# Kernel tuning notes

Hardware: AMD Instinct MI355X
Metric: run time of the kernel (lower is better)

Reference implementation:

```python
import jax, jax.numpy as jnp
import numpy as np

NB = 8            # num_blocks
D = 128           # embed_dim
D_INNER = 256     # expand=2
HEADS = 4
P = 64            # headdim
N = 32            # d_state
K = 4             # d_conv
CONV_DIM = D_INNER + 2 * N          # 320 (x, B, C streams)
D_IN_PROJ = 2 * D_INNER + 2 * N + HEADS  # 580 (z, xBC, dt)


def setup_inputs():
    key = jax.random.key(0)
    ks = iter(jax.random.split(key, 16))
    f = lambda shape, s=0.02: (jax.random.normal(next(ks), shape, jnp.float32) * s)
    B, L = 2, 4096
    return {
        'x': jax.random.normal(next(ks), (B, L, D), jnp.float32),
        'residual': jnp.zeros((B, L, D), jnp.float32),
        'ln1_w': jnp.ones((NB, D)), 'ln1_b': jnp.zeros((NB, D)),
        'ln2_w': jnp.ones((NB, D)), 'ln2_b': jnp.zeros((NB, D)),
        'fc1_w': f((NB, 4 * D, D)), 'fc1_b': jnp.zeros((NB, 4 * D)),
        'fc2_w': f((NB, D, 2 * D)), 'fc2_b': jnp.zeros((NB, D)),
        'in_proj_w': f((NB, D_IN_PROJ, D)),
        'conv_w': f((NB, CONV_DIM, K), 0.1), 'conv_b': jnp.zeros((NB, CONV_DIM)),
        'dt_bias': f((NB, HEADS), 0.1),
        'A_log': jnp.tile(jnp.log(jnp.arange(1, HEADS + 1, dtype=jnp.float32)), (NB, 1)),
        'Dp': jnp.ones((NB, HEADS)),
        'rms_w': jnp.ones((NB, D_INNER)),
        'out_proj_w': f((NB, D, D_INNER)),
        'h': 64, 'w': 64,
    }


def layernorm(x, w, b):
    mu = jnp.mean(x, -1, keepdims=True)
    var = jnp.mean((x - mu) ** 2, -1, keepdims=True)
    return (x - mu) * jax.lax.rsqrt(var + 1e-5) * w + b


def mamba2(x, in_proj_w, conv_w, conv_b, dt_bias, A_log, Dp, rms_w, out_proj_w):
    Bb, L, _ = x.shape
    zxbcdt = jnp.einsum('bld,ed->ble', x, in_proj_w)          # [B,L,580]
    z = zxbcdt[..., :D_INNER]
    xBC = zxbcdt[..., D_INNER:D_INNER + CONV_DIM]
    dt = jax.nn.softplus(zxbcdt[..., -HEADS:] + dt_bias)      # [B,L,H]
    # causal depthwise conv1d + silu
    xc = jnp.moveaxis(xBC, 1, 2)                              # [B,C,L]
    xc = jax.lax.conv_general_dilated(xc, conv_w[:, None, :], (1,), [(K - 1, 0)],
                                      feature_group_count=CONV_DIM)
    xBC = jax.nn.silu(jnp.moveaxis(xc, 1, 2) + conv_b)
    xs = xBC[..., :D_INNER].reshape(Bb, L, HEADS, P)          # [B,L,H,P]
    Bm = xBC[..., D_INNER:D_INNER + N]                        # [B,L,N]
    Cm = xBC[..., D_INNER + N:]                               # [B,L,N]
    dA = jnp.exp(dt * (-jnp.exp(A_log)))                      # [B,L,H]

    def step(hst, inp):
        dA_t, dt_t, B_t, C_t, x_t = inp
        hst = hst * dA_t[:, :, None, None] + (dt_t[:, :, None, None] * x_t[..., None]) * B_t[:, None, None, :]
        return hst, jnp.einsum('bhpn,bn->bhp', hst, C_t)

    tfirst = lambda a: jnp.moveaxis(a, 1, 0)
    h0 = jnp.zeros((Bb, HEADS, P, N), x.dtype)
    _, ys = jax.lax.scan(step, h0, (tfirst(dA), tfirst(dt), tfirst(Bm), tfirst(Cm), tfirst(xs)))
    y = jnp.moveaxis(ys, 0, 1) + Dp[None, None, :, None] * xs # [B,L,H,P]
    y = y.reshape(Bb, L, D_INNER) * jax.nn.silu(z)            # gated
    y = y * jax.lax.rsqrt(jnp.mean(y * y, -1, keepdims=True) + 1e-5) * rms_w
    return jnp.einsum('be,de->bd'.replace('b', 'bl'), y, out_proj_w)


def mlp(x, fc1_w, fc1_b, fc2_w, fc2_b):
    x12 = jnp.einsum('bld,ed->ble', x, fc1_w) + fc1_b
    x1, x2 = jnp.split(x12, 2, axis=-1)
    return jnp.einsum('ble,de->bld', jax.nn.silu(x1) * x2, fc2_w) + fc2_b


def reference(x, residual, ln1_w, ln1_b, ln2_w, ln2_b, fc1_w, fc1_b, fc2_w, fc2_b,
              in_proj_w, conv_w, conv_b, dt_bias, A_log, Dp, rms_w, out_proj_w, h, w):
    for i in range(NB):
        residual = x
        x1 = layernorm(residual, ln1_w[i], ln1_b[i])
        x_m = residual + mamba2(x1, in_proj_w[i], conv_w[i], conv_b[i], dt_bias[i],
                                A_log[i], Dp[i], rms_w[i], out_proj_w[i])
        residual = x_m
        x2 = layernorm(residual, ln2_w[i], ln2_b[i])
        x = residual + mlp(x2, fc1_w[i], fc1_b[i], fc2_w[i], fc2_b[i])
    return (x, residual)
```

## Files before the change

kernel.cpp:

```cpp
#include <hip/hip_runtime.h>
#include <hip/hip_bf16.h>
#include <cstddef>

#define NBLK 8
#define DD   128
#define DI   256
#define NH   4
#define PP   64
#define NNs  32
#define EE   580
#define BB   2
#define LLEN 4096
#define ML   (BB*LLEN)
#define SEGS 256
#define TT   16
#define GPAD 264

typedef unsigned short u16;
typedef short bf16x8 __attribute__((ext_vector_type(8)));
typedef float f32x4 __attribute__((ext_vector_type(4)));

__device__ __forceinline__ float siluf(float x){ return x / (1.f + expf(-x)); }
__device__ __forceinline__ float b2f(u16 u){ return __uint_as_float((unsigned)u << 16); }
__device__ __forceinline__ u16 f2b(float f){
    __hip_bfloat16 h = __float2bfloat16(f);
    return *reinterpret_cast<u16*>(&h);
}
__device__ __forceinline__ void ld8f(const u16* p, float* f){
    ushort4 a = *(const ushort4*)p;
    ushort4 b = *(const ushort4*)(p + 4);
    f[0]=b2f(a.x); f[1]=b2f(a.y); f[2]=b2f(a.z); f[3]=b2f(a.w);
    f[4]=b2f(b.x); f[5]=b2f(b.y); f[6]=b2f(b.z); f[7]=b2f(b.w);
}

#define IPW_N (NBLK*EE*DD)
#define OPW_N (NBLK*DD*DI)
#define F1W_N (NBLK*512*DD)
#define F2W_N (NBLK*DD*DI)
#define CVT_TOT (IPW_N+OPW_N+F1W_N+F2W_N)

__global__ __launch_bounds__(256) void cvt_weights(const float* __restrict__ ip,
                                                   const float* __restrict__ op,
                                                   const float* __restrict__ f1,
                                                   const float* __restrict__ f2,
                                                   const float* __restrict__ xin,
                                                   u16* __restrict__ dip,
                                                   u16* __restrict__ dop,
                                                   u16* __restrict__ df1,
                                                   u16* __restrict__ df2,
                                                   float* __restrict__ xout)
{
    int i = blockIdx.x * 256 + threadIdx.x;
    if (i < IPW_N)                          dip[i] = f2b(ip[i]);
    else if (i < IPW_N + OPW_N)             dop[i - IPW_N] = f2b(op[i - IPW_N]);
    else if (i < IPW_N + OPW_N + F1W_N)     df1[i - IPW_N - OPW_N] = f2b(f1[i - IPW_N - OPW_N]);
    else                                    df2[i - IPW_N - OPW_N - F1W_N] = f2b(f2[i - IPW_N - OPW_N - F1W_N]);
    if (i < ML * DD) xout[i] = xin[i];
}

__global__ __launch_bounds__(256) void inproj_ln_gemm(const float* __restrict__ X,
                                                      const float* __restrict__ lnw,
                                                      const float* __restrict__ lnb,
                                                      const u16* __restrict__ W,
                                                      u16* __restrict__ C)
{
    __shared__ __align__(16) u16 Ash[64*128];
    __shared__ __align__(16) u16 Wsh[64*128];
    __shared__ float red[64][8];
    const int tid = threadIdx.x;
    const int wave = tid >> 6, lane = tid & 63;
    const int l15 = lane & 15, quad = lane >> 4;
    const int bm = blockIdx.y * 64;
    const int bn = blockIdx.x * 64;
    const int lrow = tid >> 2, sub = tid & 3;

#pragma unroll
    for (int i = 0; i < 4; i++) {
        int k8 = sub + 4*i;
        uint4 wv = make_uint4(0u,0u,0u,0u);
        if (bn + lrow < EE)
            wv = *(const uint4*)(W + (size_t)(bn + lrow) * DD + k8*8);
        *(uint4*)&Wsh[((size_t)k8*64 + lrow) * 8] = wv;
    }

    const float* xr = X + (size_t)(bm + lrow) * DD + sub*32;
    float4 xv[8];
    float ps = 0.f, pq = 0.f;
#pragma unroll
    for (int i = 0; i < 8; i++) {
        xv[i] = *(const float4*)(xr + i*4);
        ps += xv[i].x + xv[i].y + xv[i].z + xv[i].w;
        pq += xv[i].x*xv[i].x + xv[i].y*xv[i].y + xv[i].z*xv[i].z + xv[i].w*xv[i].w;
    }
    red[lrow][sub] = ps; red[lrow][4+sub] = pq;
    __syncthreads();
    float s = red[lrow][0]+red[lrow][1]+red[lrow][2]+red[lrow][3];
    float q = red[lrow][4]+red[lrow][5]+red[lrow][6]+red[lrow][7];
    float mu = s * (1.f/DD);
    float rstd = rsqrtf(q*(1.f/DD) - mu*mu + 1e-5f);
#pragma unroll
    for (int i = 0; i < 4; i++) {
        float4 a0 = xv[2*i], a1 = xv[2*i+1];
        int c0 = sub*32 + i*8;
        u16 o[8];
        o[0] = f2b((a0.x-mu)*rstd*lnw[c0+0] + lnb[c0+0]);
        o[1] = f2b((a0.y-mu)*rstd*lnw[c0+1] + lnb[c0+1]);
        o[2] = f2b((a0.z-mu)*rstd*lnw[c0+2] + lnb[c0+2]);
        o[3] = f2b((a0.w-mu)*rstd*lnw[c0+3] + lnb[c0+3]);
        o[4] = f2b((a1.x-mu)*rstd*lnw[c0+4] + lnb[c0+4]);
        o[5] = f2b((a1.y-mu)*rstd*lnw[c0+5] + lnb[c0+5]);
        o[6] = f2b((a1.z-mu)*rstd*lnw[c0+6] + lnb[c0+6]);
        o[7] = f2b((a1.w-mu)*rstd*lnw[c0+7] + lnb[c0+7]);
        *(uint4*)&Ash[((size_t)(sub*4+i)*64 + lrow) * 8] = *(uint4*)o;
    }
    __syncthreads();

    f32x4 acc[4];
#pragma unroll
    for (int nt = 0; nt < 4; nt++) acc[nt] = (f32x4){0.f,0.f,0.f,0.f};
#pragma unroll
    for (int kk = 0; kk < 4; kk++) {
        bf16x8 af = *(const bf16x8*)&Ash[(((kk*4 + quad)*64) + wave*16 + l15) * 8];
#pragma unroll
        for (int nt = 0; nt < 4; nt++) {
            bf16x8 bfv = *(const bf16x8*)&Wsh[(((kk*4 + quad)*64) + nt*16 + l15) * 8];
            acc[nt] = __builtin_amdgcn_mfma_f32_16x16x32_bf16(af, bfv, acc[nt], 0, 0, 0);
        }
    }
#pragma unroll
    for (int nt = 0; nt < 4; nt++) {
        int n = bn + nt*16 + l15;
        if (n < EE) {
#pragma unroll
            for (int r = 0; r < 4; r++) {
                int m = bm + wave*16 + quad*4 + r;
                C[(size_t)m * EE + n] = f2b(acc[nt][r]);
            }
        }
    }
}

__global__ __launch_bounds__(256) void scan1(const u16* __restrict__ zx,
                                             const float* __restrict__ cw,
                                             const float* __restrict__ cb,
                                             const float* __restrict__ dt_bias,
                                             const float* __restrict__ A_log,
                                             u16* __restrict__ seg,
                                             float* __restrict__ segsum)
{
    __shared__ float Bsh[4][TT*NNs];
    __shared__ float dts[4][TT], das[4][TT];
    int wv = threadIdx.x >> 6;
    int p = threadIdx.x & 63;
    int sg = blockIdx.x % (SEGS/4);
    int bh = blockIdx.x / (SEGS/4);
    int h = bh % NH;
    int b = bh / NH;
    int s = sg*4 + wv;
    int l0 = s * TT;
    int row0 = b * LLEN + l0;

    float xr[TT+3];
    const u16* xcol = zx + (size_t)row0 * EE + 256 + h*64 + p;
#pragma unroll
    for (int r = 0; r < TT+3; r++) {
        int l = l0 - 3 + r;
        xr[r] = (l >= 0) ? b2f(xcol[(ptrdiff_t)(r-3) * EE]) : 0.f;
    }
    float4 wx = *(const float4*)(cw + (size_t)(h*64+p) * 4);
    float cbx = cb[h*64+p];

    if (p < NNs) {
        float br[TT+3];
        const u16* bcol = zx + (size_t)row0 * EE + 512 + p;
#pragma unroll
        for (int r = 0; r < TT+3; r++) {
            int l = l0 - 3 + r;
            br[r] = (l >= 0) ? b2f(bcol[(ptrdiff_t)(r-3) * EE]) : 0.f;
        }
        float4 wb = *(const float4*)(cw + (size_t)(256+p) * 4);
        float cbb = cb[256+p];
#pragma unroll
        for (int t = 0; t < TT; t++)
            Bsh[wv][t*NNs + p] = siluf(cbb + wb.x*br[t] + wb.y*br[t+1] + wb.z*br[t+2] + wb.w*br[t+3]);
    }
    if (p < TT) {
        float v = b2f(zx[(size_t)(row0+p)*EE + (EE-NH) + h]) + dt_bias[h];
        float dt = (v > 20.f) ? v : log1pf(expf(v));
        dts[wv][p] = dt;
        das[wv][p] = expf(-expf(A_log[h]) * dt);
    }
    __syncthreads();

    float hreg[NNs];
#pragma unroll
    for (int n = 0; n < NNs; n++) hreg[n] = 0.f;
    float sdt = 0.f;
#pragma unroll
    for (int t = 0; t < TT; t++) {
        float dA = das[wv][t];
        float dt = dts[wv][t];
        float xv = siluf(cbx + wx.x*xr[t] + wx.y*xr[t+1] + wx.z*xr[t+2] + wx.w*xr[t+3]);
        float dtx = dt * xv;
#pragma unroll
        for (int n4 = 0; n4 < 8; n4++) {
            float4 Bv = *(const float4*)&Bsh[wv][t*NNs + n4*4];
            hreg[n4*4+0] = fmaf(hreg[n4*4+0], dA, dtx * Bv.x);
            hreg[n4*4+1] = fmaf(hreg[n4*4+1], dA, dtx * Bv.y);
            hreg[n4*4+2] = fmaf(hreg[n4*4+2], dA, dtx * Bv.z);
            hreg[n4*4+3] = fmaf(hreg[n4*4+3], dA, dtx * Bv.w);
        }
        sdt += dt;
    }
    int bidg = bh * SEGS + s;
    u16* dst = seg + ((size_t)bidg * PP + p) * NNs;
#pragma unroll
    for (int n8 = 0; n8 < 4; n8++) {
        u16 ob[8];
#pragma unroll
        for (int j = 0; j < 8; j++) ob[j] = f2b(hreg[n8*8 + j]);
        *(uint4*)(dst + n8*8) = *(uint4*)ob;
    }
    if (p == 0) segsum[bidg] = sdt;
}

__global__ __launch_bounds__(256) void scan2(u16* __restrict__ seg,
                                             const float* __restrict__ segsum,
                                             const float* __restrict__ A_log)
{
    int bh = blockIdx.x >> 3;
    int chunk = blockIdx.x & 7;
    int h = bh % NH;
    int entry = chunk * 256 + threadIdx.x;
    float negA = -expf(A_log[h]);
    float hs = 0.f;
    const float* ss = segsum + bh * SEGS;
    u16* base = seg + (size_t)bh * SEGS * (PP * NNs) + entry;
    for (int j0 = 0; j0 < SEGS; j0 += 16) {
        float e[16], a[16];
#pragma unroll
        for (int k = 0; k < 16; k++) {
            a[k] = ss[j0 + k];
            e[k] = b2f(base[(size_t)(j0 + k) * (PP * NNs)]);
        }
#pragma unroll
        for (int k = 0; k < 16; k++) {
            float Aj = expf(negA * a[k]);
            base[(size_t)(j0 + k) * (PP * NNs)] = f2b(hs);
            hs = fmaf(Aj, hs, e[k]);
        }
    }
}

__global__ __launch_bounds__(256) void scan3(const u16* __restrict__ zx,
                                             const float* __restrict__ cw,
                                             const float* __restrict__ cb,
                                             const float* __restrict__ dt_bias,
                                             const float* __restrict__ A_log,
                                             const u16* __restrict__ seg,
                                             const float* __restrict__ Dp,
                                             u16* __restrict__ y)
{
    __shared__ float BCsh[4][TT*64];
    __shared__ float dts[4][TT], das[4][TT];
    int wv = threadIdx.x >> 6;
    int p = threadIdx.x & 63;
    int sg = blockIdx.x % (SEGS/4);
    int bh = blockIdx.x / (SEGS/4);
    int h = bh % NH;
    int b = bh / NH;
    int s = sg*4 + wv;
    int l0 = s * TT;
    int row0 = b * LLEN + l0;

    float xr[TT+3];
    const u16* xcol = zx + (size_t)row0 * EE + 256 + h*64 + p;
#pragma unroll
    for (int r = 0; r < TT+3; r++) {
        int l = l0 - 3 + r;
        xr[r] = (l >= 0) ? b2f(xcol[(ptrdiff_t)(r-3) * EE]) : 0.f;
    }
    float4 wx = *(const float4*)(cw + (size_t)(h*64+p) * 4);
    float cbx = cb[h*64+p];

    {
        float br[TT+3];
        const u16* bcol = zx + (size_t)row0 * EE + 512 + p;
#pragma unroll
        for (int r = 0; r < TT+3; r++) {
            int l = l0 - 3 + r;
            br[r] = (l >= 0) ? b2f(bcol[(ptrdiff_t)(r-3) * EE]) : 0.f;
        }
        float4 wb = *(const float4*)(cw + (size_t)(256+p) * 4);
        float cbb = cb[256+p];
#pragma unroll
        for (int t = 0; t < TT; t++)
            BCsh[wv][t*64 + p] = siluf(cbb + wb.x*br[t] + wb.y*br[t+1] + wb.z*br[t+2] + wb.w*br[t+3]);
    }
    if (p < TT) {
        float v = b2f(zx[(size_t)(row0+p)*EE + (EE-NH) + h]) + dt_bias[h];
        float dt = (v > 20.f) ? v : log1pf(expf(v));
        dts[wv][p] = dt;
        das[wv][p] = expf(-expf(A_log[h]) * dt);
    }

    float hreg[NNs];
    int bidg = bh * SEGS + s;
    const u16* src = seg + ((size_t)bidg * PP + p) * NNs;
#pragma unroll
    for (int n8 = 0; n8 < 4; n8++) {
        float f[8];
        ld8f(src + n8*8, f);
#pragma unroll
        for (int j = 0; j < 8; j++) hreg[n8*8 + j] = f[j];
    }
    float dp = Dp[h];
    __syncthreads();

#pragma unroll
    for (int t = 0; t < TT; t++) {
        float dA = das[wv][t];
        float dt = dts[wv][t];
        float xv = siluf(cbx + wx.x*xr[t] + wx.y*xr[t+1] + wx.z*xr[t+2] + wx.w*xr[t+3]);
        float dtx = dt * xv;
        float acc = 0.f;
#pragma unroll
        for (int n4 = 0; n4 < 8; n4++) {
            float4 Bv = *(const float4*)&BCsh[wv][t*64 + n4*4];
            float4 Cv = *(const float4*)&BCsh[wv][t*64 + 32 + n4*4];
            hreg[n4*4+0] = fmaf(hreg[n4*4+0], dA, dtx * Bv.x);
            hreg[n4*4+1] = fmaf(hreg[n4*4+1], dA, dtx * Bv.y);
            hreg[n4*4+2] = fmaf(hreg[n4*4+2], dA, dtx * Bv.z);
            hreg[n4*4+3] = fmaf(hreg[n4*4+3], dA, dtx * Bv.w);
            acc = fmaf(hreg[n4*4+0], Cv.x, acc);
            acc = fmaf(hreg[n4*4+1], Cv.y, acc);
            acc = fmaf(hreg[n4*4+2], Cv.z, acc);
            acc = fmaf(hreg[n4*4+3], Cv.w, acc);
        }
        y[(size_t)(row0 + t) * DI + h*PP + p] = f2b(acc + dp * xv);
    }
}

__global__ __launch_bounds__(256) void grms_outproj_gemm(const u16* __restrict__ Y,
                                                         const u16* __restrict__ Z,
                                                         const float* __restrict__ rmsw,
                                                         const u16* __restrict__ W,
                                                         const float* __restrict__ resid,
                                                         float* __restrict__ C)
{
    __shared__ __align__(16) u16 Ash[32*256];
    __shared__ __align__(16) u16 Wsh[64*256];
    __shared__ float red[32][8];
    __shared__ float rl[32];
    const int tid = threadIdx.x;
    const int wave = tid >> 6, lane = tid & 63;
    const int l15 = lane & 15, quad = lane >> 4;
    const int rt = wave & 1, nq = wave >> 1;
    const int bm = blockIdx.y * 32;
    const int bn = blockIdx.x * 64;

    {
        int wrow = tid >> 2, ksub = tid & 3;
#pragma unroll
        for (int i = 0; i < 8; i++) {
            int k8 = ksub + 4*i;
            uint4 wv = *(const uint4*)(W + (size_t)(bn + wrow) * DI + k8*8);
            *(uint4*)&Wsh[((size_t)k8*64 + wrow) * 8] = wv;
        }
    }

    int lrow = tid >> 3, sub = tid & 7;
    const u16* yr = Y + (size_t)(bm + lrow) * DI + sub*32;
    const u16* zr = Z + (size_t)(bm + lrow) * EE + sub*32;
    float pq = 0.f;
#pragma unroll
    for (int i = 0; i < 4; i++) {
        float yv[8], zv[8];
        ld8f(yr + i*8, yv);
        ld8f(zr + i*8, zv);
        int c0 = sub*32 + i*8;
        u16 o[8];
#pragma unroll
        for (int j = 0; j < 8; j++) {
            float g = yv[j] * siluf(zv[j]);
            pq += g*g;
            o[j] = f2b(g * rmsw[c0 + j]);
        }
        *(uint4*)&Ash[((size_t)(sub*4 + i)*32 + lrow) * 8] = *(uint4*)o;
    }
    red[lrow][sub] = pq;
    __syncthreads();
    if (sub == 0) {
        float qq = 0.f;
#pragma unroll
        for (int j = 0; j < 8; j++) qq += red[lrow][j];
        rl[lrow] = rsqrtf(qq * (1.f/DI) + 1e-5f);
    }
    __syncthreads();

    f32x4 acc[2];
    acc[0] = (f32x4){0.f,0.f,0.f,0.f};
    acc[1] = (f32x4){0.f,0.f,0.f,0.f};
#pragma unroll
    for (int kk = 0; kk < 8; kk++) {
        bf16x8 af = *(const bf16x8*)&Ash[(((kk*4 + quad)*32) + rt*16 + l15) * 8];
#pragma unroll
        for (int nt = 0; nt < 2; nt++) {
            bf16x8 bfv = *(const bf16x8*)&Wsh[(((kk*4 + quad)*64) + nq*32 + nt*16 + l15) * 8];
            acc[nt] = __builtin_amdgcn_mfma_f32_16x16x32_bf16(af, bfv, acc[nt], 0, 0, 0);
        }
    }
#pragma unroll
    for (int nt = 0; nt < 2; nt++) {
        int n = bn + nq*32 + nt*16 + l15;
#pragma unroll
        for (int r = 0; r < 4; r++) {
            int lm = rt*16 + quad*4 + r;
            int m = bm + lm;
            C[(size_t)m * DD + n] = acc[nt][r] * rl[lm] + resid[(size_t)m * DD + n];
        }
    }
}

__global__ __launch_bounds__(512) void mlp_fused(const float* __restrict__ Xm,
                                                 const float* __restrict__ lnw,
                                                 const float* __restrict__ lnb,
                                                 const u16* __restrict__ W1,
                                                 const float* __restrict__ b1,
                                                 const u16* __restrict__ W2,
                                                 const float* __restrict__ b2,
                                                 float* __restrict__ Out,
                                                 float* __restrict__ out2)
{
    __shared__ __align__(16) u16 Ash[32*128];
    __shared__ __align__(16) u16 Wsh[128*128];
    __shared__ __align__(16) u16 Gsh[32*GPAD];
    __shared__ float red[32][32];
    const int tid = threadIdx.x;
    const int wv = tid >> 6, lane = tid & 63;
    const int l15 = lane & 15, quad = lane >> 4;
    const int mt = wv & 1, ng = wv >> 1;
    const int bm = blockIdx.x * 32;

    {
        int lrow = tid >> 4, sub = tid & 15;
        const float* xr = Xm + (size_t)(bm + lrow) * DD + sub*8;
        float4 x0 = *(const float4*)xr;
        float4 x1 = *(const float4*)(xr + 4);
        float ps = x0.x+x0.y+x0.z+x0.w + x1.x+x1.y+x1.z+x1.w;
        float pq = x0.x*x0.x+x0.y*x0.y+x0.z*x0.z+x0.w*x0.w
                 + x1.x*x1.x+x1.y*x1.y+x1.z*x1.z+x1.w*x1.w;
        red[lrow][sub] = ps; red[lrow][16+sub] = pq;
        __syncthreads();
        float s = 0.f, q = 0.f;
#pragma unroll
        for (int j = 0; j < 16; j++) { s += red[lrow][j]; q += red[lrow][16+j]; }
        float mu = s * (1.f/DD);
        float rstd = rsqrtf(q*(1.f/DD) - mu*mu + 1e-5f);
        int c0 = sub*8;
        float xa[8] = {x0.x,x0.y,x0.z,x0.w,x1.x,x1.y,x1.z,x1.w};
        u16 o[8];
#pragma unroll
        for (int j = 0; j < 8; j++)
            o[j] = f2b((xa[j]-mu)*rstd*lnw[c0+j] + lnb[c0+j]);
        *(uint4*)&Ash[((size_t)sub*32 + lrow) * 8] = *(uint4*)o;
    }
    __syncthreads();

    bf16x8 afr[4];
#pragma unroll
    for (int kk = 0; kk < 4; kk++)
        afr[kk] = *(const bf16x8*)&Ash[(((kk*4 + quad)*32) + mt*16 + l15) * 8];

    for (int p = 0; p < 4; p++) {
        __syncthreads();
        {
            int wrow = tid >> 2, ksub = tid & 3;
            int r1 = (wrow < 64) ? (p*64 + wrow) : (256 + p*64 + wrow - 64);
#pragma unroll
            for (int i = 0; i < 4; i++) {
                int k8 = ksub + 4*i;
                uint4 wvv = *(const uint4*)(W1 + (size_t)r1 * DD + k8*8);
                *(uint4*)&Wsh[((size_t)k8*128 + wrow) * 8] = wvv;
            }
        }
        __syncthreads();
        f32x4 aa = (f32x4){0.f,0.f,0.f,0.f};
        f32x4 bb = (f32x4){0.f,0.f,0.f,0.f};
#pragma unroll
        for (int kk = 0; kk < 4; kk++) {
            bf16x8 b1v = *(const bf16x8*)&Wsh[(((kk*4 + quad)*128) + ng*16 + l15) * 8];
            bf16x8 b2v = *(const bf16x8*)&Wsh[(((kk*4 + quad)*128) + 64 + ng*16 + l15) * 8];
            aa = __builtin_amdgcn_mfma_f32_16x16x32_bf16(afr[kk], b1v, aa, 0, 0, 0);
            bb = __builtin_amdgcn_mfma_f32_16x16x32_bf16(afr[kk], b2v, bb, 0, 0, 0);
        }
        int n1 = p*64 + ng*16 + l15;
        float ba = b1[n1];
        float bbv = b1[256 + n1];
#pragma unroll
        for (int r = 0; r < 4; r++) {
            float a = aa[r] + ba;
            float bq = bb[r] + bbv;
            int m = mt*16 + quad*4 + r;
            Gsh[m*GPAD + n1] = f2b(siluf(a) * bq);
        }
    }

    f32x4 acc2[2];
    acc2[0] = (f32x4){0.f,0.f,0.f,0.f};
    acc2[1] = (f32x4){0.f,0.f,0.f,0.f};
    for (int kh = 0; kh < 2; kh++) {
        __syncthreads();
        {
            int wrow = tid >> 2, ksub = tid & 3;
#pragma unroll
            for (int i = 0; i < 4; i++) {
                int k8 = ksub + 4*i;
                uint4 wvv = *(const uint4*)(W2 + (size_t)wrow * DI + kh*128 + k8*8);
                *(uint4*)&Wsh[((size_t)k8*128 + wrow) * 8] = wvv;
            }
        }
        __syncthreads();
#pragma unroll
        for (int kk = 0; kk < 4; kk++) {
            bf16x8 af = *(const bf16x8*)&Gsh[(mt*16 + l15)*GPAD + kh*128 + kk*32 + quad*8];
#pragma unroll
            for (int nt = 0; nt < 2; nt++) {
                bf16x8 bfv = *(const bf16x8*)&Wsh[(((kk*4 + quad)*128) + ng*32 + nt*16 + l15) * 8];
                acc2[nt] = __builtin_amdgcn_mfma_f32_16x16x32_bf16(af, bfv, acc2[nt], 0, 0, 0);
            }
        }
    }
#pragma unroll
    for (int nt = 0; nt < 2; nt++) {
        int n = ng*32 + nt*16 + l15;
        float bv = b2[n];
#pragma unroll
        for (int r = 0; r < 4; r++) {
            int m = bm + mt*16 + quad*4 + r;
            float xmv = Xm[(size_t)m * DD + n];
            float v = acc2[nt][r] + bv + xmv;
            Out[(size_t)m * DD + n] = v;
            if (out2) {
                out2[(size_t)m * DD + n] = v;
                out2[(size_t)ML*DD + (size_t)m * DD + n] = xmv;
            }
        }
    }
}

extern "C" void kernel_launch(void* const* d_in, const int* in_sizes, int n_in,
                              void* d_out, int out_size, void* d_ws, size_t ws_size,
                              hipStream_t stream)
{
    (void)in_sizes; (void)n_in; (void)out_size; (void)ws_size;
    const float* x_in      = (const float*)d_in[0];
    const float* ln1_w     = (const float*)d_in[2];
    const float* ln1_b     = (const float*)d_in[3];
    const float* ln2_w     = (const float*)d_in[4];
    const float* ln2_b     = (const float*)d_in[5];
    const float* fc1_w     = (const float*)d_in[6];
    const float* fc1_b     = (const float*)d_in[7];
    const float* fc2_w     = (const float*)d_in[8];
    const float* fc2_b     = (const float*)d_in[9];
    const float* in_proj_w = (const float*)d_in[10];
    const float* conv_w    = (const float*)d_in[11];
    const float* conv_b    = (const float*)d_in[12];
    const float* dt_bias   = (const float*)d_in[13];
    const float* A_log     = (const float*)d_in[14];
    const float* Dp        = (const float*)d_in[15];
    const float* rms_w     = (const float*)d_in[16];
    const float* out_proj_w= (const float*)d_in[17];

    float* ws = (float*)d_ws;
    size_t o = 0;
    float* bufX    = ws + o; o += (size_t)ML * DD;
    float* bufXm   = ws + o; o += (size_t)ML * DD;
    float* bufSegA = ws + o; o += (size_t)BB * NH * SEGS;
    u16* bufSeg   = (u16*)(ws + o); o += (size_t)BB * NH * SEGS * PP * NNs / 2;
    u16* bufBigH  = (u16*)(ws + o); o += ((size_t)ML * EE + 1) / 2;
    u16* bufYH    = (u16*)(ws + o); o += (size_t)ML * DI / 2;
    u16* wIpH     = (u16*)(ws + o); o += (IPW_N + 1) / 2;
    u16* wOpH     = (u16*)(ws + o); o += (OPW_N + 1) / 2;
    u16* wF1H     = (u16*)(ws + o); o += (F1W_N + 1) / 2;
    u16* wF2H     = (u16*)(ws + o); o += (F2W_N + 1) / 2;

    cvt_weights<<<CVT_TOT/256, 256, 0, stream>>>(in_proj_w, out_proj_w, fc1_w, fc2_w,
                                                 x_in, wIpH, wOpH, wF1H, wF2H, bufX);

    for (int i = 0; i < NBLK; i++) {
        const float* ln1wi = ln1_w + i * DD;
        const float* ln1bi = ln1_b + i * DD;
        const float* ln2wi = ln2_w + i * DD;
        const float* ln2bi = ln2_b + i * DD;
        const float* cwi   = conv_w + (size_t)i * 320 * 4;
        const float* cbi   = conv_b + (size_t)i * 320;
        const float* dtbi  = dt_bias + i * NH;
        const float* ali   = A_log + i * NH;
        const float* dpi   = Dp + i * NH;
        const float* rwi   = rms_w + (size_t)i * DI;
        const float* f1bi  = fc1_b + (size_t)i * 512;
        const float* f2bi  = fc2_b + (size_t)i * DD;
        const u16* ipwi = wIpH + (size_t)i * EE * DD;
        const u16* opwi = wOpH + (size_t)i * DD * DI;
        const u16* f1wi = wF1H + (size_t)i * 512 * DD;
        const u16* f2wi = wF2H + (size_t)i * DD * DI;

        inproj_ln_gemm<<<dim3(10, ML/64), 256, 0, stream>>>(bufX, ln1wi, ln1bi, ipwi, bufBigH);
        scan1<<<BB*NH*(SEGS/4), 256, 0, stream>>>(bufBigH, cwi, cbi, dtbi, ali, bufSeg, bufSegA);
        scan2<<<BB*NH*8, 256, 0, stream>>>(bufSeg, bufSegA, ali);
        scan3<<<BB*NH*(SEGS/4), 256, 0, stream>>>(bufBigH, cwi, cbi, dtbi, ali, bufSeg, dpi, bufYH);
        grms_outproj_gemm<<<dim3(2, ML/32), 256, 0, stream>>>(bufYH, bufBigH, rwi, opwi,
                                                              bufX, bufXm);
        mlp_fused<<<ML/32, 512, 0, stream>>>(bufXm, ln2wi, ln2bi, f1wi, f1bi,
                                             f2wi, f2bi, bufX,
                                             (i == NBLK-1) ? (float*)d_out : nullptr);
    }
}
```

Before: 837.9 us.

## Fuse gating and RMS statistics into scan3, reuse LN tile across N tiles

scan3 is restructured so each block handles one segment across all four heads. It now applies the silu(z) gate and computes the per-row RMS sum of squares with wave reductions, writing a gated, rms-weighted bf16 G plus a per-row rsqrt factor. The out-projection GEMM then just loads G and the factor instead of re-reading y and z, and the in-projection kernel computes LayerNorm once per row tile for two N tiles (grid halved). The MLP kernel also caches the Xm residual tile in shared memory rather than re-reading it from global. The cost is more shared memory and fewer blocks in the in-projection and scan kernels.

Result: slower. 1.786 ms (+113.1%).

```diff
diff --git a/kernel.cpp b/kernel.cpp
--- a/kernel.cpp
+++ b/kernel.cpp
@@ -32,6 +32,11 @@
     f[0]=b2f(a.x); f[1]=b2f(a.y); f[2]=b2f(a.z); f[3]=b2f(a.w);
     f[4]=b2f(b.x); f[5]=b2f(b.y); f[6]=b2f(b.z); f[7]=b2f(b.w);
 }
+__device__ __forceinline__ float waveReduceSum(float v){
+#pragma unroll
+    for (int off = 32; off > 0; off >>= 1) v += __shfl_xor(v, off, 64);
+    return v;
+}
 
 #define IPW_N (NBLK*EE*DD)
 #define OPW_N (NBLK*DD*DI)
@@ -71,17 +76,7 @@
     const int wave = tid >> 6, lane = tid & 63;
     const int l15 = lane & 15, quad = lane >> 4;
     const int bm = blockIdx.y * 64;
-    const int bn = blockIdx.x * 64;
     const int lrow = tid >> 2, sub = tid & 3;
-
-#pragma unroll
-    for (int i = 0; i < 4; i++) {
-        int k8 = sub + 4*i;
-        uint4 wv = make_uint4(0u,0u,0u,0u);
-        if (bn + lrow < EE)
-            wv = *(const uint4*)(W + (size_t)(bn + lrow) * DD + k8*8);
-        *(uint4*)&Wsh[((size_t)k8*64 + lrow) * 8] = wv;
-    }
 
     const float* xr = X + (size_t)(bm + lrow) * DD + sub*32;
     float4 xv[8];
@@ -113,28 +108,42 @@
         o[7] = f2b((a1.w-mu)*rstd*lnw[c0+7] + lnb[c0+7]);
         *(uint4*)&Ash[((size_t)(sub*4+i)*64 + lrow) * 8] = *(uint4*)o;
     }
-    __syncthreads();
-
-    f32x4 acc[4];
-#pragma unroll
-    for (int nt = 0; nt < 4; nt++) acc[nt] = (f32x4){0.f,0.f,0.f,0.f};
-#pragma unroll
-    for (int kk = 0; kk < 4; kk++) {
-        bf16x8 af = *(const bf16x8*)&Ash[(((kk*4 + quad)*64) + wave*16 + l15) * 8];
+
+#pragma unroll 1
+    for (int t2 = 0; t2 < 2; t2++) {
+        int bn = (blockIdx.x * 2 + t2) * 64;
+        __syncthreads();
+#pragma unroll
+        for (int i = 0; i < 4; i++) {
+            int k8 = sub + 4*i;
+            uint4 wv = make_uint4(0u,0u,0u,0u);
+            if (bn + lrow < EE)
+                wv = *(const uint4*)(W + (size_t)(bn + lrow) * DD + k8*8);
+            *(uint4*)&Wsh[((size_t)k8*64 + lrow) * 8] = wv;
+        }
+        __syncthreads();
+
+        f32x4 acc[4];
+#pragma unroll
+        for (int nt = 0; nt < 4; nt++) acc[nt] = (f32x4){0.f,0.f,0.f,0.f};
+#pragma unroll
+        for (int kk = 0; kk < 4; kk++) {
+            bf16x8 af = *(const bf16x8*)&Ash[(((kk*4 + quad)*64) + wave*16 + l15) * 8];
+#pragma unroll
+            for (int nt = 0; nt < 4; nt++) {
+                bf16x8 bfv = *(const bf16x8*)&Wsh[(((kk*4 + quad)*64) + nt*16 + l15) * 8];
+                acc[nt] = __builtin_amdgcn_mfma_f32_16x16x32_bf16(af, bfv, acc[nt], 0, 0, 0);
+            }
+        }
 #pragma unroll
         for (int nt = 0; nt < 4; nt++) {
-            bf16x8 bfv = *(const bf16x8*)&Wsh[(((kk*4 + quad)*64) + nt*16 + l15) * 8];
-            acc[nt] = __builtin_amdgcn_mfma_f32_16x16x32_bf16(af, bfv, acc[nt], 0, 0, 0);
-        }
-    }
-#pragma unroll
-    for (int nt = 0; nt < 4; nt++) {
-        int n = bn + nt*16 + l15;
-        if (n < EE) {
-#pragma unroll
-            for (int r = 0; r < 4; r++) {
-                int m = bm + wave*16 + quad*4 + r;
-                C[(size_t)m * EE + n] = f2b(acc[nt][r]);
+            int n = bn + nt*16 + l15;
+            if (n < EE) {
+#pragma unroll
+                for (int r = 0; r < 4; r++) {
+                    int m = bm + wave*16 + quad*4 + r;
+                    C[(size_t)m * EE + n] = f2b(acc[nt][r]);
+                }
             }
         }
     }
@@ -252,82 +261,85 @@
     }
 }
 
-__global__ __launch_bounds__(256) void scan3(const u16* __restrict__ zx,
-                                             const float* __restrict__ cw,
-                                             const float* __restrict__ cb,
-                                             const float* __restrict__ dt_bias,
-                                             const float* __restrict__ A_log,
-                                             const u16* __restrict__ seg,
-                                             const float* __restrict__ Dp,
-                                             u16* __restrict__ y)
-{
-    __shared__ float BCsh[4][TT*64];
-    __shared__ float dts[4][TT], das[4][TT];
-    int wv = threadIdx.x >> 6;
-    int p = threadIdx.x & 63;
-    int sg = blockIdx.x % (SEGS/4);
-    int bh = blockIdx.x / (SEGS/4);
-    int h = bh % NH;
-    int b = bh / NH;
-    int s = sg*4 + wv;
-    int l0 = s * TT;
-    int row0 = b * LLEN + l0;
+__global__ __launch_bounds__(256) void scan3_g(const u16* __restrict__ zx,
+                                               const float* __restrict__ cw,
+                                               const float* __restrict__ cb,
+                                               const float* __restrict__ dt_bias,
+                                               const float* __restrict__ A_log,
+                                               const u16* __restrict__ seg,
+                                               const float* __restrict__ Dp,
+                                               const float* __restrict__ rmsw,
+                                               u16* __restrict__ G,
+                                               float* __restrict__ rlg)
+{
+    __shared__ float BCsh[4*1024];
+    __shared__ float dts[4*16], das[4*16];
+    __shared__ float part[16*4];
+    const int tid = threadIdx.x;
+    const int wv = tid >> 6, p = tid & 63;
+    const int s = blockIdx.x % SEGS;
+    const int b = blockIdx.x / SEGS;
+    const int h = wv;
+    const int l0 = s * TT;
+    const int row0 = b * LLEN + l0;
 
     float xr[TT+3];
-    const u16* xcol = zx + (size_t)row0 * EE + 256 + h*64 + p;
+    const u16* xcol = zx + (size_t)row0*EE + 256 + h*64 + p;
 #pragma unroll
     for (int r = 0; r < TT+3; r++) {
         int l = l0 - 3 + r;
-        xr[r] = (l >= 0) ? b2f(xcol[(ptrdiff_t)(r-3) * EE]) : 0.f;
-    }
-    float4 wx = *(const float4*)(cw + (size_t)(h*64+p) * 4);
+        xr[r] = (l >= 0) ? b2f(xcol[(ptrdiff_t)(r-3)*EE]) : 0.f;
+    }
+    float4 wx = *(const float4*)(cw + (size_t)(h*64+p)*4);
     float cbx = cb[h*64+p];
-
     {
         float br[TT+3];
-        const u16* bcol = zx + (size_t)row0 * EE + 512 + p;
+        const u16* bcol = zx + (size_t)row0*EE + 512 + p;
 #pragma unroll
         for (int r = 0; r < TT+3; r++) {
             int l = l0 - 3 + r;
-            br[r] = (l >= 0) ? b2f(bcol[(ptrdiff_t)(r-3) * EE]) : 0.f;
-        }
-        float4 wb = *(const float4*)(cw + (size_t)(256+p) * 4);
+            br[r] = (l >= 0) ? b2f(bcol[(ptrdiff_t)(r-3)*EE]) : 0.f;
+        }
+        float4 wb = *(const float4*)(cw + (size_t)(256+p)*4);
         float cbb = cb[256+p];
 #pragma unroll
         for (int t = 0; t < TT; t++)
-            BCsh[wv][t*64 + p] = siluf(cbb + wb.x*br[t] + wb.y*br[t+1] + wb.z*br[t+2] + wb.w*br[t+3]);
+            BCsh[wv*1024 + t*64 + p] = siluf(cbb + wb.x*br[t] + wb.y*br[t+1] + wb.z*br[t+2] + wb.w*br[t+3]);
     }
     if (p < TT) {
         float v = b2f(zx[(size_t)(row0+p)*EE + (EE-NH) + h]) + dt_bias[h];
         float dt = (v > 20.f) ? v : log1pf(expf(v));
-        dts[wv][p] = dt;
-        das[wv][p] = expf(-expf(A_log[h]) * dt);
-    }
-
+        dts[wv*16 + p] = dt;
+        das[wv*16 + p] = expf(-expf(A_log[h]) * dt);
+    }
     float hreg[NNs];
-    int bidg = bh * SEGS + s;
-    const u16* src = seg + ((size_t)bidg * PP + p) * NNs;
-#pragma unroll
-    for (int n8 = 0; n8 < 4; n8++) {
-        float f[8];
-        ld8f(src + n8*8, f);
-#pragma unroll
-        for (int j = 0; j < 8; j++) hreg[n8*8 + j] = f[j];
-    }
-    float dp = Dp[h];
+    {
+        int bidg = (b*NH + h)*SEGS + s;
+        const u16* src = seg + ((size_t)bidg*PP + p)*NNs;
+#pragma unroll
+        for (int n8 = 0; n8 < 4; n8++) {
+            float f[8];
+            ld8f(src + n8*8, f);
+#pragma unroll
+            for (int j = 0; j < 8; j++) hreg[n8*8 + j] = f[j];
+        }
+    }
+    float dpv = Dp[h];
+    const u16* zcol = zx + (size_t)row0*EE + h*64 + p;
     __syncthreads();
 
+    float gs[TT];
 #pragma unroll
     for (int t = 0; t < TT; t++) {
-        float dA = das[wv][t];
-        float dt = dts[wv][t];
+        float dA = das[wv*16 + t];
+        float dt = dts[wv*16 + t];
         float xv = siluf(cbx + wx.x*xr[t] + wx.y*xr[t+1] + wx.z*xr[t+2] + wx.w*xr[t+3]);
         float dtx = dt * xv;
         float acc = 0.f;
 #pragma unroll
         for (int n4 = 0; n4 < 8; n4++) {
-            float4 Bv = *(const float4*)&BCsh[wv][t*64 + n4*4];
-            float4 Cv = *(const float4*)&BCsh[wv][t*64 + 32 + n4*4];
+            float4 Bv = *(const float4*)&BCsh[wv*1024 + t*64 + n4*4];
+            float4 Cv = *(const float4*)&BCsh[wv*1024 + t*64 + 32 + n4*4];
             hreg[n4*4+0] = fmaf(hreg[n4*4+0], dA, dtx * Bv.x);
             hreg[n4*4+1] = fmaf(hreg[n4*4+1], dA, dtx * Bv.y);
             hreg[n4*4+2] = fmaf(hreg[n4*4+2], dA, dtx * Bv.z);
@@ -337,20 +349,34 @@
             acc = fmaf(hreg[n4*4+2], Cv.z, acc);
             acc = fmaf(hreg[n4*4+3], Cv.w, acc);
         }
-        y[(size_t)(row0 + t) * DI + h*PP + p] = f2b(acc + dp * xv);
-    }
-}
-
-__global__ __launch_bounds__(256) void grms_outproj_gemm(const u16* __restrict__ Y,
-                                                         const u16* __restrict__ Z,
-                                                         const float* __restrict__ rmsw,
+        float y = acc + dpv * xv;
+        gs[t] = y * siluf(b2f(zcol[(ptrdiff_t)t * EE]));
+    }
+    {
+        int c = h*64 + p;
+        float rw = rmsw[c];
+#pragma unroll
+        for (int t = 0; t < TT; t++) {
+            float w = waveReduceSum(gs[t]*gs[t]);
+            if (p == 0) part[t*4 + wv] = w;
+            G[(size_t)(row0 + t)*DI + c] = f2b(gs[t] * rw);
+        }
+    }
+    __syncthreads();
+    if (tid < TT) {
+        float qq = part[tid*4+0] + part[tid*4+1] + part[tid*4+2] + part[tid*4+3];
+        rlg[row0 + tid] = rsqrtf(qq * (1.f/DI) + 1e-5f);
+    }
+}
+
+__global__ __launch_bounds__(256) void grms_outproj_gemm(const u16* __restrict__ G,
+                                                         const float* __restrict__ rlg,
                                                          const u16* __restrict__ W,
                                                          const float* __restrict__ resid,
                                                          float* __restrict__ C)
 {
     __shared__ __align__(16) u16 Ash[32*256];
     __shared__ __align__(16) u16 Wsh[64*256];
-    __shared__ float red[32][8];
     __shared__ float rl[32];
     const int tid = threadIdx.x;
     const int wave = tid >> 6, lane = tid & 63;
@@ -368,34 +394,12 @@
             *(uint4*)&Wsh[((size_t)k8*64 + wrow) * 8] = wv;
         }
     }
-
     int lrow = tid >> 3, sub = tid & 7;
-    const u16* yr = Y + (size_t)(bm + lrow) * DI + sub*32;
-    const u16* zr = Z + (size_t)(bm + lrow) * EE + sub*32;
-    float pq = 0.f;
-#pragma unroll
-    for (int i = 0; i < 4; i++) {
-        float yv[8], zv[8];
-        ld8f(yr + i*8, yv);
-        ld8f(zr + i*8, zv);
-        int c0 = sub*32 + i*8;
-        u16 o[8];
-#pragma unroll
-        for (int j = 0; j < 8; j++) {
-            float g = yv[j] * siluf(zv[j]);
-            pq += g*g;
-            o[j] = f2b(g * rmsw[c0 + j]);
-        }
-        *(uint4*)&Ash[((size_t)(sub*4 + i)*32 + lrow) * 8] = *(uint4*)o;
-    }
-    red[lrow][sub] = pq;
-    __syncthreads();
-    if (sub == 0) {
-        float qq = 0.f;
-#pragma unroll
-        for (int j = 0; j < 8; j++) qq += red[lrow][j];
-        rl[lrow] = rsqrtf(qq * (1.f/DI) + 1e-5f);
-    }
+    const u16* gr = G + (size_t)(bm + lrow) * DI + sub*32;
+#pragma unroll
+    for (int i = 0; i < 4; i++)
+        *(uint4*)&Ash[((size_t)(sub*4 + i)*32 + lrow) * 8] = *(const uint4*)(gr + i*8);
+    if (sub == 0) rl[lrow] = rlg[bm + lrow];
     __syncthreads();
 
     f32x4 acc[2];
@@ -435,6 +439,7 @@
     __shared__ __align__(16) u16 Ash[32*128];
     __shared__ __align__(16) u16 Wsh[128*128];
     __shared__ __align__(16) u16 Gsh[32*GPAD];
+    __shared__ float Xsh[32*132];
     __shared__ float red[32][32];
     const int tid = threadIdx.x;
     const int wv = tid >> 6, lane = tid & 63;
@@ -447,6 +452,8 @@
         const float* xr = Xm + (size_t)(bm + lrow) * DD + sub*8;
         float4 x0 = *(const float4*)xr;
         float4 x1 = *(const float4*)(xr + 4);
+        *(float4*)&Xsh[lrow*132 + sub*8]     = x0;
+        *(float4*)&Xsh[lrow*132 + sub*8 + 4] = x1;
         float ps = x0.x+x0.y+x0.z+x0.w + x1.x+x1.y+x1.z+x1.w;
         float pq = x0.x*x0.x+x0.y*x0.y+x0.z*x0.z+x0.w*x0.w
                  + x1.x*x1.x+x1.y*x1.y+x1.z*x1.z+x1.w*x1.w;
@@ -537,8 +544,9 @@
         float bv = b2[n];
 #pragma unroll
         for (int r = 0; r < 4; r++) {
-            int m = bm + mt*16 + quad*4 + r;
-            float xmv = Xm[(size_t)m * DD + n];
+            int lm = mt*16 + quad*4 + r;
+            int m = bm + lm;
+            float xmv = Xsh[lm*132 + n];
             float v = acc2[nt][r] + bv + xmv;
             Out[(size_t)m * DD + n] = v;
             if (out2) {
@@ -577,9 +585,10 @@
     float* bufX    = ws + o; o += (size_t)ML * DD;
     float* bufXm   = ws + o; o += (size_t)ML * DD;
     float* bufSegA = ws + o; o += (size_t)BB * NH * SEGS;
+    float* bufRL   = ws + o; o += (size_t)ML;
     u16* bufSeg   = (u16*)(ws + o); o += (size_t)BB * NH * SEGS * PP * NNs / 2;
     u16* bufBigH  = (u16*)(ws + o); o += ((size_t)ML * EE + 1) / 2;
-    u16* bufYH    = (u16*)(ws + o); o += (size_t)ML * DI / 2;
+    u16* bufGH    = (u16*)(ws + o); o += (size_t)ML * DI / 2;
     u16* wIpH     = (u16*)(ws + o); o += (IPW_N + 1) / 2;
     u16* wOpH     = (u16*)(ws + o); o += (OPW_N + 1) / 2;
     u16* wF1H     = (u16*)(ws + o); o += (F1W_N + 1) / 2;
@@ -606,11 +615,12 @@
         const u16* f1wi = wF1H + (size_t)i * 512 * DD;
         const u16* f2wi = wF2H + (size_t)i * DD * DI;
 
-        inproj_ln_gemm<<<dim3(10, ML/64), 256, 0, stream>>>(bufX, ln1wi, ln1bi, ipwi, bufBigH);
+        inproj_ln_gemm<<<dim3(5, ML/64), 256, 0, stream>>>(bufX, ln1wi, ln1bi, ipwi, bufBigH);
         scan1<<<BB*NH*(SEGS/4), 256, 0, stream>>>(bufBigH, cwi, cbi, dtbi, ali, bufSeg, bufSegA);
         scan2<<<BB*NH*8, 256, 0, stream>>>(bufSeg, bufSegA, ali);
-        scan3<<<BB*NH*(SEGS/4), 256, 0, stream>>>(bufBigH, cwi, cbi, dtbi, ali, bufSeg, dpi, bufYH);
-        grms_outproj_gemm<<<dim3(2, ML/32), 256, 0, stream>>>(bufYH, bufBigH, rwi, opwi,
+        scan3_g<<<BB*SEGS, 256, 0, stream>>>(bufBigH, cwi, cbi, dtbi, ali, bufSeg, dpi,
+                                             rwi, bufGH, bufRL);
+        grms_outproj_gemm<<<dim3(2, ML/32), 256, 0, stream>>>(bufGH, bufRL, opwi,
                                                               bufX, bufXm);
         mlp_fused<<<ML/32, 512, 0, stream>>>(bufXm, ln2wi, ln2bi, f1wi, f1bi,
                                              f2wi, f2bi, bufX,
```
